# Performance work log

Hardware: AMD Instinct MI355X
Metric: run time of the kernel (lower is better)

## Reference

```python
import jax, jax.numpy as jnp
import numpy as np


def _bce_logits(x, t):
    # numerically stable BCEWithLogits (pos_weight=1), elementwise
    return jnp.maximum(x, 0.0) - x * t + jnp.log1p(jnp.exp(-jnp.abs(x)))


def _ciou(box1, box2, eps=1e-9):
    # box1, box2: [n,4] in (cx, cy, w, h); matches bbox_iou(..., x1y1x2y2=False, CIoU=True)
    b1x1, b1x2 = box1[:, 0] - box1[:, 2] / 2, box1[:, 0] + box1[:, 2] / 2
    b1y1, b1y2 = box1[:, 1] - box1[:, 3] / 2, box1[:, 1] + box1[:, 3] / 2
    b2x1, b2x2 = box2[:, 0] - box2[:, 2] / 2, box2[:, 0] + box2[:, 2] / 2
    b2y1, b2y2 = box2[:, 1] - box2[:, 3] / 2, box2[:, 1] + box2[:, 3] / 2
    inter = (jnp.clip(jnp.minimum(b1x2, b2x2) - jnp.maximum(b1x1, b2x1), 0.0)
             * jnp.clip(jnp.minimum(b1y2, b2y2) - jnp.maximum(b1y1, b2y1), 0.0))
    w1, h1 = b1x2 - b1x1, b1y2 - b1y1 + eps
    w2, h2 = b2x2 - b2x1, b2y2 - b2y1 + eps
    union = w1 * h1 + w2 * h2 - inter + eps
    iou = inter / union
    cw = jnp.maximum(b1x2, b2x2) - jnp.minimum(b1x1, b2x1)
    ch = jnp.maximum(b1y2, b2y2) - jnp.minimum(b1y1, b2y1)
    c2 = cw ** 2 + ch ** 2 + eps
    rho2 = ((b2x1 + b2x2 - b1x1 - b1x2) ** 2 + (b2y1 + b2y2 - b1y1 - b1y2) ** 2) / 4.0
    v = (4.0 / jnp.pi ** 2) * (jnp.arctan(w2 / h2) - jnp.arctan(w1 / h1)) ** 2
    alpha = jax.lax.stop_gradient(v / (1.0 + eps - iou + v))  # torch.no_grad()
    return iou - (rho2 / c2 + v * alpha)


def _layer_loss(preds, targets, anchors, li):
    # preds: [B, na, H, W, 5+nc]; targets: [nt,6]; anchors: [n_layers, na, 2]
    B, na, H, W, C = preds.shape
    nt = targets.shape[0]
    ai = jnp.arange(na, dtype=preds.dtype)
    # targets.repeat(na,1,1) with anchor index appended -> [na, nt, 7]
    t7 = jnp.concatenate([jnp.broadcast_to(targets[None], (na, nt, 6)),
                          jnp.broadcast_to(ai[:, None, None], (na, nt, 1))], axis=2)
    gain = jnp.array([1.0, 1.0, W, H, W, H, 1.0], dtype=preds.dtype)
    t = t7 * gain
    # anchor-ratio filter: max(r, 1/r).max(-1) < 4 (as boolean mask instead of fancy-index)
    r = t[:, :, 4:6] / anchors[li][:, None, :]                  # [na, nt, 2]
    mask = jnp.max(jnp.maximum(r, 1.0 / r), axis=2) < 4.0       # [na, nt]
    tf = t.reshape(na * nt, 7)
    m = mask.reshape(-1)
    mf = m.astype(preds.dtype)
    b = tf[:, 0].astype(jnp.int32)
    c = tf[:, 1].astype(jnp.int32)
    gxy = tf[:, 2:4]
    gwh = tf[:, 4:6]
    gij = gxy.astype(jnp.int32)  # .long() truncation (coords >= 0)
    gi = jnp.clip(gij[:, 0], 0, W - 1)
    gj = jnp.clip(gij[:, 1], 0, H - 1)
    a = tf[:, 6].astype(jnp.int32)
    # faithful to original: anch = anchors[a] then forward takes [range(n), a] => anchors[a, a]
    anch = anchors[a, a]
    # img_ids = unique(batch ids).flip(); with full 0..B-1 coverage lookup == B-1-b
    match = (B - 1) - b
    ps = preds[match, a, gj, gi]                                # [na*nt, C] gather
    pxy = jax.nn.sigmoid(ps[:, :2])
    pwh = jnp.exp(ps[:, 2:4]) * anch
    pbox = jnp.concatenate([pxy, pwh], axis=1)
    tbox = jnp.concatenate([gxy - gij.astype(gxy.dtype), gwh], axis=1)
    iou = _ciou(pbox, tbox)
    nvalid = jnp.maximum(mf.sum(), 1.0)
    lbox = ((1.0 - iou) * mf).sum() / nvalid                    # mean over matched targets
    # scatter detached clamped iou into tobj; invalid rows get OOB batch idx -> dropped
    scatter_b = jnp.where(m, match, B)
    tobj = jnp.zeros((B, na, H, W), preds.dtype).at[scatter_b, a, gj, gi].set(
        jax.lax.stop_gradient(jnp.clip(iou, 0.0)) * mf)
    nc = C - 5
    t1h = jax.nn.one_hot(c, nc, dtype=preds.dtype)
    lcls = (_bce_logits(ps[:, 5:], t1h) * mf[:, None]).sum() / (nvalid * nc)
    lobj = _bce_logits(preds[..., 4], tobj).mean()
    return lbox, lobj, lcls


def setup_inputs() -> dict:
    key = jax.random.key(0)
    ks = jax.random.split(key, 6)
    p0 = jax.random.normal(ks[0], (16, 3, 80, 80, 85), jnp.float32)
    p1 = jax.random.normal(ks[1], (16, 3, 40, 40, 85), jnp.float32)
    p2 = jax.random.normal(ks[2], (16, 3, 20, 20, 85), jnp.float32)
    nt, B = 300, 16
    img = (jnp.arange(nt) % B).astype(jnp.float32)  # every batch id present
    cls = jax.random.randint(ks[3], (nt,), 0, 80).astype(jnp.float32)
    xy = jax.random.uniform(ks[4], (nt, 2), minval=0.05, maxval=0.95)
    wh = jax.random.uniform(ks[5], (nt, 2), minval=0.02, maxval=0.2)
    targets = jnp.concatenate([img[:, None], cls[:, None], xy, wh], axis=1)
    anchors = jnp.array([[[1.25, 1.625], [2.0, 3.75], [4.125, 2.875]],
                         [[1.875, 3.8125], [3.875, 2.8125], [3.6875, 7.4375]],
                         [[3.625, 2.8125], [4.875, 6.1875], [11.65625, 10.1875]]],
                        dtype=jnp.float32)
    return {"p0": p0, "p1": p1, "p2": p2, "targets": targets, "anchors": anchors}


def reference(p0, p1, p2, targets, anchors):
    lb = lo = lc = 0.0
    for li, p in enumerate((p0, p1, p2)):
        a_, b_, c_ = _layer_loss(p, targets, anchors, li)
        lb = lb + a_
        lo = lo + b_
        lc = lc + c_
    lbox = lb * 0.05
    lobj = lo * 1.0
    lcls = lc * 0.5
    loss = lbox + lobj + lcls
    stats = jnp.stack([lbox, lobj, lcls, loss])
    return (jnp.reshape(loss, (1,)), stats)
```

## Files before the change

kernel.cpp:

```cpp
#include <hip/hip_runtime.h>
#include <math.h>

#define NT    300
#define NA    3
#define BATCH 16
#define NCLS  80
#define CCH   85
#define NBO   394
#define NBT   675
#define NBLK  (NBO + NBT)


__device__ __forceinline__ float softplusf(float x) {
    return fmaxf(x, 0.f) + log1pf(expf(-fabsf(x)));
}

__device__ __forceinline__ double block_reduce(double v, double* red) {
    #pragma unroll
    for (int off = 32; off > 0; off >>= 1) v += __shfl_down(v, off, 64);
    const int wid = threadIdx.x >> 6, lane = threadIdx.x & 63;
    if (lane == 0) red[wid] = v;
    __syncthreads();
    double r = (threadIdx.x < 4) ? red[threadIdx.x] : 0.0;
    r += __shfl_down(r, 2, 64);
    r += __shfl_down(r, 1, 64);
    __syncthreads();
    return r;
}

__global__ __launch_bounds__(256) void main_kernel(
    const float* __restrict__ p0, const float* __restrict__ p1,
    const float* __restrict__ p2,
    const float* __restrict__ targets, const float* __restrict__ anchors,
    char* __restrict__ ws)
{
    __shared__ double red[4];
    __shared__ double acc[4][4];

    double* obj_part = (double*)ws;
    double* tgt_part = (double*)(ws + 3200);

    if (blockIdx.x < NBO) {
        const int ob = blockIdx.x;
        int li, bb;
        if (ob < 300)      { li = 0; bb = ob; }
        else if (ob < 375) { li = 1; bb = ob - 300; }
        else               { li = 2; bb = ob - 375; }
        const float* p = (li == 0) ? p0 : ((li == 1) ? p1 : p2);
        const int N = (BATCH * NA * 6400) >> (2*li);

        float s = 0.f;
        #pragma unroll
        for (int k = 0; k < 4; ++k) {
            const int idx = bb * 1024 + k * 256 + threadIdx.x;
            if (idx < N) s += softplusf(p[(size_t)idx * CCH + 4]);
        }
        const double t = block_reduce((double)s, red);
        if (threadIdx.x == 0) obj_part[ob] = t;
        return;
    }

    const int tb   = blockIdx.x - NBO;
    const int gr   = tb * 4 + (threadIdx.x >> 6);
    const int lane = threadIdx.x & 63;
    const int li   = gr / (NA * NT);
    const int r    = gr - li * (NA * NT);
    const int a    = r / NT;
    const int ti   = r - a * NT;
    const float* p = (li == 0) ? p0 : ((li == 1) ? p1 : p2);
    const int W = 80 >> li, H = W;

    const float img = targets[ti*6 + 0];
    const float cls = targets[ti*6 + 1];
    const float tx  = targets[ti*6 + 2] * (float)W;
    const float ty  = targets[ti*6 + 3] * (float)H;
    const float tw  = targets[ti*6 + 4] * (float)W;
    const float th  = targets[ti*6 + 5] * (float)H;

    const float ax = anchors[(li*3 + a)*2 + 0];
    const float ay = anchors[(li*3 + a)*2 + 1];
    const float rx = tw / ax, ry = th / ay;
    const float mr = fmaxf(fmaxf(rx, 1.f/rx), fmaxf(ry, 1.f/ry));
    const bool  mask = mr < 4.f;
    const float mf = mask ? 1.f : 0.f;

    const int b = (int)img;
    const int c = (int)cls;
    const int gij_x = (int)tx;
    const int gij_y = (int)ty;
    const int gi = min(max(gij_x, 0), W - 1);
    const int gj = min(max(gij_y, 0), H - 1);

    bool beaten = false;
    for (int tj = ti + 1 + lane; tj < NT; tj += 64) {
        const float img_j = targets[tj*6 + 0];
        const float xj = targets[tj*6 + 2] * (float)W;
        const float yj = targets[tj*6 + 3] * (float)H;
        const float wj = targets[tj*6 + 4] * (float)W;
        const float hj = targets[tj*6 + 5] * (float)H;
        const float rxj = wj / ax, ryj = hj / ay;
        const float mrj = fmaxf(fmaxf(rxj, 1.f/rxj), fmaxf(ryj, 1.f/ryj));
        if (mrj < 4.f && img_j == img) {
            const int gi_j = min(max((int)xj, 0), W - 1);
            const int gj_j = min(max((int)yj, 0), H - 1);
            if (gi_j == gi && gj_j == gj) beaten = true;
        }
    }
    const bool winner = mask && !__any(beaten);

    const float anch_x = anchors[(a*3 + a)*2 + 0];
    const float anch_y = anchors[(a*3 + a)*2 + 1];

    const int match = BATCH - 1 - b;
    const int cell  = ((match*NA + a)*H + gj)*W + gi;
    const float* ps = p + (size_t)cell * CCH;

    const float x1 = ps[lane];
    const float x2 = (lane < CCH - 64) ? ps[64 + lane] : 0.f;

    const float s0   = __shfl(x1, 0);
    const float s1   = __shfl(x1, 1);
    const float s2   = __shfl(x1, 2);
    const float s3   = __shfl(x1, 3);
    const float objx = __shfl(x1, 4);

    const int ch = 5 + c;
    float contrib = (lane >= 5) ? softplusf(x1) : 0.f;
    if (lane < CCH - 64) contrib += softplusf(x2);
    if (lane == ch) contrib -= x1;
    if (ch >= 64 && lane == ch - 64) contrib -= x2;
    #pragma unroll
    for (int off = 32; off > 0; off >>= 1)
        contrib += __shfl_down(contrib, off, 64);

    const float pxx = 1.f / (1.f + expf(-s0));
    const float pyy = 1.f / (1.f + expf(-s1));
    const float pw  = expf(s2) * anch_x;
    const float ph  = expf(s3) * anch_y;
    const float fx  = tx - (float)gij_x;
    const float fy  = ty - (float)gij_y;

    const float eps = 1e-9f;
    const float b1x1 = pxx - pw*0.5f, b1x2 = pxx + pw*0.5f;
    const float b1y1 = pyy - ph*0.5f, b1y2 = pyy + ph*0.5f;
    const float b2x1 = fx - tw*0.5f,  b2x2 = fx + tw*0.5f;
    const float b2y1 = fy - th*0.5f,  b2y2 = fy + th*0.5f;
    float iw = fminf(b1x2, b2x2) - fmaxf(b1x1, b2x1); iw = fmaxf(iw, 0.f);
    float ih = fminf(b1y2, b2y2) - fmaxf(b1y1, b2y1); ih = fmaxf(ih, 0.f);
    const float inter = iw * ih;
    const float w1 = b1x2 - b1x1, h1 = b1y2 - b1y1 + eps;
    const float w2 = b2x2 - b2x1, h2 = b2y2 - b2y1 + eps;
    const float uni = w1*h1 + w2*h2 - inter + eps;
    const float iou = inter / uni;
    const float cw  = fmaxf(b1x2, b2x2) - fminf(b1x1, b2x1);
    const float chh = fmaxf(b1y2, b2y2) - fminf(b1y1, b2y1);
    const float c2 = cw*cw + chh*chh + eps;
    const float dx = b2x1 + b2x2 - b1x1 - b1x2;
    const float dy = b2y1 + b2y2 - b1y1 - b1y2;
    const float rho2 = (dx*dx + dy*dy) * 0.25f;
    const float dat = atanf(w2/h2) - atanf(w1/h1);
    const float v = 0.40528473456935108577f * dat * dat;
    const float alpha = v / (1.f + eps - iou + v);
    const float ciou = iou - (rho2/c2 + v*alpha);

    if (lane == 0) {
        const int wid = threadIdx.x >> 6;
        acc[wid][0] = (double)((1.f - ciou) * mf);
        acc[wid][1] = (double)(contrib * mf);
        acc[wid][2] = (double)mf;
        acc[wid][3] = winner ? (double)(objx * fmaxf(ciou, 0.f)) : 0.0;
    }
    __syncthreads();
    if (threadIdx.x < 4) {
        tgt_part[tb*4 + threadIdx.x] =
            acc[0][threadIdx.x] + acc[1][threadIdx.x] +
            acc[2][threadIdx.x] + acc[3][threadIdx.x];
    }
}

__global__ __launch_bounds__(256) void final_kernel(
    const char* __restrict__ ws, float* __restrict__ out)
{
    __shared__ double red[4];
    const double* obj_part = (const double*)ws;
    const double* tgt_part = (const double*)(ws + 3200);

    double so[3] = {0,0,0};
    double lb[3] = {0,0,0}, lc[3] = {0,0,0}, nv[3] = {0,0,0}, co[3] = {0,0,0};

    for (int bk = threadIdx.x; bk < NBO; bk += 256) {
        const int l = (bk < 300) ? 0 : ((bk < 375) ? 1 : 2);
        so[l] += obj_part[bk];
    }
    for (int tb = threadIdx.x; tb < NBT; tb += 256) {
        const int l = (tb < 225) ? 0 : ((tb < 450) ? 1 : 2);
        lb[l] += tgt_part[tb*4 + 0];
        lc[l] += tgt_part[tb*4 + 1];
        nv[l] += tgt_part[tb*4 + 2];
        co[l] += tgt_part[tb*4 + 3];
    }

    double rsum[15];
    #pragma unroll
    for (int l = 0; l < 3; ++l) {
        rsum[l*5 + 0] = block_reduce(lb[l], red);
        rsum[l*5 + 1] = block_reduce(lc[l], red);
        rsum[l*5 + 2] = block_reduce(co[l], red);
        rsum[l*5 + 3] = block_reduce(nv[l], red);
        rsum[l*5 + 4] = block_reduce(so[l], red);
    }

    if (threadIdx.x == 0) {
        double lbox = 0.0, lobj = 0.0, lcls = 0.0;
        for (int l = 0; l < 3; ++l) {
            const double nvv = fmax(rsum[l*5 + 3], 1.0);
            lbox += rsum[l*5 + 0] / nvv;
            lcls += rsum[l*5 + 1] / (nvv * (double)NCLS);
            const double N = (double)((BATCH * NA * 6400) >> (2*l));
            lobj += (rsum[l*5 + 4] - rsum[l*5 + 2]) / N;
        }
        lbox *= 0.05;
        lcls *= 0.5;
        const double loss = lbox + lobj + lcls;
        out[0] = (float)loss;
        out[1] = (float)lbox;
        out[2] = (float)lobj;
        out[3] = (float)lcls;
        out[4] = (float)loss;
    }
}

extern "C" void kernel_launch(void* const* d_in, const int* in_sizes, int n_in,
                              void* d_out, int out_size, void* d_ws, size_t ws_size,
                              hipStream_t stream) {
    const float* p0      = (const float*)d_in[0];
    const float* p1      = (const float*)d_in[1];
    const float* p2      = (const float*)d_in[2];
    const float* targets = (const float*)d_in[3];
    const float* anchors = (const float*)d_in[4];

    main_kernel<<<NBLK, 256, 0, stream>>>(p0, p1, p2, targets, anchors,
                                          (char*)d_ws);
    final_kernel<<<1, 256, 0, stream>>>((const char*)d_ws, (float*)d_out);
}
```

Measured before the change: 178.0 us.

## Fuse objectness, target and final reduction into one cooperative kernel

Merges the two kernel launches into a single cooperative kernel of 675 blocks. Each block handles both an objectness chunk and four target rows, then a grid-wide sync lets block 0 perform the final reduction. The aim is to remove the second launch and the extra idle blocks, at the cost of a grid barrier and the constraint that all blocks fit co-resident. The previous two-kernel path is kept as a fallback if the cooperative launch fails. Target loads in the pairwise loop are also vectorized to float2.

```diff
diff --git a/kernel.cpp b/kernel.cpp
--- a/kernel.cpp
+++ b/kernel.cpp
@@ -1,14 +1,18 @@
 #include <hip/hip_runtime.h>
+#include <hip/hip_cooperative_groups.h>
 #include <math.h>
+
+namespace cg = cooperative_groups;
 
 #define NT    300
 #define NA    3
 #define BATCH 16
 #define NCLS  80
 #define CCH   85
+#define NCHUNK 394
+#define NBLK   675
 #define NBO   394
 #define NBT   675
-#define NBLK  (NBO + NBT)
 
 
 __device__ __forceinline__ float softplusf(float x) {
@@ -28,45 +32,23 @@
     return r;
 }
 
-__global__ __launch_bounds__(256) void main_kernel(
+__device__ __forceinline__ double wred(double v) {
+    #pragma unroll
+    for (int off = 32; off > 0; off >>= 1) v += __shfl_down(v, off, 64);
+    return v;
+}
+
+__device__ __forceinline__ void target_row(
+    int gr, int lane,
     const float* __restrict__ p0, const float* __restrict__ p1,
     const float* __restrict__ p2,
     const float* __restrict__ targets, const float* __restrict__ anchors,
-    char* __restrict__ ws)
+    float out4[4])
 {
-    __shared__ double red[4];
-    __shared__ double acc[4][4];
-
-    double* obj_part = (double*)ws;
-    double* tgt_part = (double*)(ws + 3200);
-
-    if (blockIdx.x < NBO) {
-        const int ob = blockIdx.x;
-        int li, bb;
-        if (ob < 300)      { li = 0; bb = ob; }
-        else if (ob < 375) { li = 1; bb = ob - 300; }
-        else               { li = 2; bb = ob - 375; }
-        const float* p = (li == 0) ? p0 : ((li == 1) ? p1 : p2);
-        const int N = (BATCH * NA * 6400) >> (2*li);
-
-        float s = 0.f;
-        #pragma unroll
-        for (int k = 0; k < 4; ++k) {
-            const int idx = bb * 1024 + k * 256 + threadIdx.x;
-            if (idx < N) s += softplusf(p[(size_t)idx * CCH + 4]);
-        }
-        const double t = block_reduce((double)s, red);
-        if (threadIdx.x == 0) obj_part[ob] = t;
-        return;
-    }
-
-    const int tb   = blockIdx.x - NBO;
-    const int gr   = tb * 4 + (threadIdx.x >> 6);
-    const int lane = threadIdx.x & 63;
-    const int li   = gr / (NA * NT);
-    const int r    = gr - li * (NA * NT);
-    const int a    = r / NT;
-    const int ti   = r - a * NT;
+    const int li = gr / (NA * NT);
+    const int r  = gr - li * (NA * NT);
+    const int a  = r / NT;
+    const int ti = r - a * NT;
     const float* p = (li == 0) ? p0 : ((li == 1) ? p1 : p2);
     const int W = 80 >> li, H = W;
 
@@ -93,14 +75,14 @@
 
     bool beaten = false;
     for (int tj = ti + 1 + lane; tj < NT; tj += 64) {
-        const float img_j = targets[tj*6 + 0];
-        const float xj = targets[tj*6 + 2] * (float)W;
-        const float yj = targets[tj*6 + 3] * (float)H;
-        const float wj = targets[tj*6 + 4] * (float)W;
-        const float hj = targets[tj*6 + 5] * (float)H;
+        const float2 tA = *(const float2*)(targets + tj*6 + 0);
+        const float2 tB = *(const float2*)(targets + tj*6 + 2);
+        const float2 tC = *(const float2*)(targets + tj*6 + 4);
+        const float xj = tB.x * (float)W, yj = tB.y * (float)H;
+        const float wj = tC.x * (float)W, hj = tC.y * (float)H;
         const float rxj = wj / ax, ryj = hj / ay;
         const float mrj = fmaxf(fmaxf(rxj, 1.f/rxj), fmaxf(ryj, 1.f/ryj));
-        if (mrj < 4.f && img_j == img) {
+        if (mrj < 4.f && tA.x == img) {
             const int gi_j = min(max((int)xj, 0), W - 1);
             const int gj_j = min(max((int)yj, 0), H - 1);
             if (gi_j == gi && gj_j == gj) beaten = true;
@@ -163,19 +145,153 @@
     const float alpha = v / (1.f + eps - iou + v);
     const float ciou = iou - (rho2/c2 + v*alpha);
 
+    out4[0] = (1.f - ciou) * mf;
+    out4[1] = contrib * mf;
+    out4[2] = mf;
+    out4[3] = winner ? objx * fmaxf(ciou, 0.f) : 0.f;
+}
+
+__global__ __launch_bounds__(256, 3) void fused_kernel(
+    const float* __restrict__ p0, const float* __restrict__ p1,
+    const float* __restrict__ p2,
+    const float* __restrict__ targets, const float* __restrict__ anchors,
+    char* __restrict__ ws, float* __restrict__ out)
+{
+    __shared__ double red[4];
+    __shared__ double acc[4][4];
+
+    double* obj_part = (double*)ws;
+    double* tgt_part = (double*)(ws + 3200);
+
+    const int tb   = blockIdx.x;
+    const int wid  = threadIdx.x >> 6;
+    const int lane = threadIdx.x & 63;
+
+    float s = 0.f;
+    if (tb < NCHUNK) {
+        int li, bb;
+        if (tb < 300)      { li = 0; bb = tb; }
+        else if (tb < 375) { li = 1; bb = tb - 300; }
+        else               { li = 2; bb = tb - 375; }
+        const float* p = (li == 0) ? p0 : ((li == 1) ? p1 : p2);
+        const int N = (BATCH * NA * 6400) >> (2*li);
+        #pragma unroll
+        for (int k = 0; k < 4; ++k) {
+            const int idx = bb * 1024 + k * 256 + threadIdx.x;
+            if (idx < N) s += softplusf(p[(size_t)idx * CCH + 4]);
+        }
+    }
+
+    float o4[4];
+    target_row(tb*4 + wid, lane, p0, p1, p2, targets, anchors, o4);
     if (lane == 0) {
-        const int wid = threadIdx.x >> 6;
-        acc[wid][0] = (double)((1.f - ciou) * mf);
-        acc[wid][1] = (double)(contrib * mf);
-        acc[wid][2] = (double)mf;
-        acc[wid][3] = winner ? (double)(objx * fmaxf(ciou, 0.f)) : 0.0;
-    }
+        acc[wid][0] = (double)o4[0];
+        acc[wid][1] = (double)o4[1];
+        acc[wid][2] = (double)o4[2];
+        acc[wid][3] = (double)o4[3];
+    }
+
+    const double t = block_reduce((double)s, red);
+    if (tb < NCHUNK && threadIdx.x == 0) obj_part[tb] = t;
+
     __syncthreads();
-    if (threadIdx.x < 4) {
+    if (threadIdx.x < 4)
         tgt_part[tb*4 + threadIdx.x] =
             acc[0][threadIdx.x] + acc[1][threadIdx.x] +
             acc[2][threadIdx.x] + acc[3][threadIdx.x];
-    }
+
+    cg::this_grid().sync();
+
+    if (blockIdx.x == 0 && threadIdx.x < 64) {
+        double so0=0,so1=0,so2=0;
+        double lb0=0,lb1=0,lb2=0, lc0=0,lc1=0,lc2=0;
+        double nv0=0,nv1=0,nv2=0, co0=0,co1=0,co2=0;
+        for (int bk = lane; bk < NCHUNK; bk += 64) {
+            const double v = obj_part[bk];
+            if (bk < 300)      so0 += v;
+            else if (bk < 375) so1 += v;
+            else               so2 += v;
+        }
+        for (int q = lane; q < NBLK; q += 64) {
+            const double a0 = tgt_part[q*4+0], a1 = tgt_part[q*4+1];
+            const double a2 = tgt_part[q*4+2], a3 = tgt_part[q*4+3];
+            if (q < 225)      { lb0+=a0; lc0+=a1; nv0+=a2; co0+=a3; }
+            else if (q < 450) { lb1+=a0; lc1+=a1; nv1+=a2; co1+=a3; }
+            else              { lb2+=a0; lc2+=a1; nv2+=a2; co2+=a3; }
+        }
+        so0=wred(so0); so1=wred(so1); so2=wred(so2);
+        lb0=wred(lb0); lb1=wred(lb1); lb2=wred(lb2);
+        lc0=wred(lc0); lc1=wred(lc1); lc2=wred(lc2);
+        nv0=wred(nv0); nv1=wred(nv1); nv2=wred(nv2);
+        co0=wred(co0); co1=wred(co1); co2=wred(co2);
+        if (lane == 0) {
+            const double so[3]={so0,so1,so2}, lb[3]={lb0,lb1,lb2};
+            const double lc[3]={lc0,lc1,lc2}, nv[3]={nv0,nv1,nv2};
+            const double co[3]={co0,co1,co2};
+            double lbox = 0.0, lobj = 0.0, lcls = 0.0;
+            #pragma unroll
+            for (int l = 0; l < 3; ++l) {
+                const double nvv = fmax(nv[l], 1.0);
+                lbox += lb[l] / nvv;
+                lcls += lc[l] / (nvv * (double)NCLS);
+                const double N = (double)((BATCH * NA * 6400) >> (2*l));
+                lobj += (so[l] - co[l]) / N;
+            }
+            lbox *= 0.05;
+            lcls *= 0.5;
+            const double loss = lbox + lobj + lcls;
+            out[0] = (float)loss;
+            out[1] = (float)lbox;
+            out[2] = (float)lobj;
+            out[3] = (float)lcls;
+            out[4] = (float)loss;
+        }
+    }
+}
+
+__global__ __launch_bounds__(256) void main_kernel(
+    const float* __restrict__ p0, const float* __restrict__ p1,
+    const float* __restrict__ p2,
+    const float* __restrict__ targets, const float* __restrict__ anchors,
+    char* __restrict__ ws)
+{
+    __shared__ double red[4];
+    __shared__ double acc[4][4];
+    double* obj_part = (double*)ws;
+    double* tgt_part = (double*)(ws + 3200);
+
+    if (blockIdx.x < NBO) {
+        const int ob = blockIdx.x;
+        int li, bb;
+        if (ob < 300)      { li = 0; bb = ob; }
+        else if (ob < 375) { li = 1; bb = ob - 300; }
+        else               { li = 2; bb = ob - 375; }
+        const float* p = (li == 0) ? p0 : ((li == 1) ? p1 : p2);
+        const int N = (BATCH * NA * 6400) >> (2*li);
+        float s = 0.f;
+        #pragma unroll
+        for (int k = 0; k < 4; ++k) {
+            const int idx = bb * 1024 + k * 256 + threadIdx.x;
+            if (idx < N) s += softplusf(p[(size_t)idx * CCH + 4]);
+        }
+        const double t = block_reduce((double)s, red);
+        if (threadIdx.x == 0) obj_part[ob] = t;
+        return;
+    }
+    const int tb = blockIdx.x - NBO;
+    float o4[4];
+    target_row(tb*4 + (threadIdx.x >> 6), threadIdx.x & 63,
+               p0, p1, p2, targets, anchors, o4);
+    const int wid = threadIdx.x >> 6;
+    if ((threadIdx.x & 63) == 0) {
+        acc[wid][0] = (double)o4[0]; acc[wid][1] = (double)o4[1];
+        acc[wid][2] = (double)o4[2]; acc[wid][3] = (double)o4[3];
+    }
+    __syncthreads();
+    if (threadIdx.x < 4)
+        tgt_part[tb*4 + threadIdx.x] =
+            acc[0][threadIdx.x] + acc[1][threadIdx.x] +
+            acc[2][threadIdx.x] + acc[3][threadIdx.x];
 }
 
 __global__ __launch_bounds__(256) void final_kernel(
@@ -187,7 +303,6 @@
 
     double so[3] = {0,0,0};
     double lb[3] = {0,0,0}, lc[3] = {0,0,0}, nv[3] = {0,0,0}, co[3] = {0,0,0};
-
     for (int bk = threadIdx.x; bk < NBO; bk += 256) {
         const int l = (bk < 300) ? 0 : ((bk < 375) ? 1 : 2);
         so[l] += obj_part[bk];
@@ -199,7 +314,6 @@
         nv[l] += tgt_part[tb*4 + 2];
         co[l] += tgt_part[tb*4 + 3];
     }
-
     double rsum[15];
     #pragma unroll
     for (int l = 0; l < 3; ++l) {
@@ -209,7 +323,6 @@
         rsum[l*5 + 3] = block_reduce(nv[l], red);
         rsum[l*5 + 4] = block_reduce(so[l], red);
     }
-
     if (threadIdx.x == 0) {
         double lbox = 0.0, lobj = 0.0, lcls = 0.0;
         for (int l = 0; l < 3; ++l) {
@@ -238,8 +351,17 @@
     const float* p2      = (const float*)d_in[2];
     const float* targets = (const float*)d_in[3];
     const float* anchors = (const float*)d_in[4];
-
-    main_kernel<<<NBLK, 256, 0, stream>>>(p0, p1, p2, targets, anchors,
-                                          (char*)d_ws);
-    final_kernel<<<1, 256, 0, stream>>>((const char*)d_ws, (float*)d_out);
-}
+    char*  ws  = (char*)d_ws;
+    float* out = (float*)d_out;
+
+    void* args[7] = {(void*)&p0, (void*)&p1, (void*)&p2,
+                     (void*)&targets, (void*)&anchors,
+                     (void*)&ws, (void*)&out};
+    const hipError_t e = hipLaunchCooperativeKernel(
+        fused_kernel, dim3(NBLK), dim3(256), args, 0, stream);
+    if (e != hipSuccess) {
+        main_kernel<<<NBO + NBT, 256, 0, stream>>>(p0, p1, p2, targets,
+                                                   anchors, ws);
+        final_kernel<<<1, 256, 0, stream>>>(ws, out);
+    }
+}
```

Result: slower. 265.1 us (+48.9%).
